# Performance work log

Measured on AMD Instinct MI355X. Metric: run time of the kernel, lower is better.

Reference implementation:

```python
import jax, jax.numpy as jnp
import numpy as np

EMBED = 1024
HEADS = 16
B, T = 2, 1024


def setup_inputs() -> dict:
    key = jax.random.key(0)
    k1, k2 = jax.random.split(key)
    x = jax.random.normal(k1, (B, T, EMBED), dtype=jnp.float32)
    # causal mask: True positions are masked to -inf (torch masked_fill semantics)
    mask = jnp.triu(jnp.ones((T, T), dtype=bool), k=1)
    weight = jax.random.normal(k2, (HEADS * EMBED, EMBED), dtype=jnp.float32)
    return {"x": x, "mask": mask, "weight": weight}


def reference(x, mask, weight):
    b, t, c = x.shape
    h = weight.shape[0] // c  # num_heads
    # split channels into heads: (b, h, t, head_dim)
    y = x.reshape(b, t, h, c // h).transpose(0, 2, 1, 3)
    # per-head scores (b, h, t, t)
    s = jnp.einsum('bhtk,bhsk->bhts', y, y)
    # mask BEFORE scaling, then scale by sqrt(num_heads) (not head_dim!)
    s = jnp.where(mask, -jnp.inf, s)
    p = jax.nn.softmax(s / jnp.sqrt(jnp.asarray(h, dtype=s.dtype)), axis=-1)
    # V is raw x broadcast across heads: (b, h, t, c)
    o = jnp.einsum('bhts,bsc->bhtc', p, x)
    # concat heads -> (b, t, h*c), final linear
    o = o.transpose(0, 2, 1, 3).reshape(b, t, h * c)
    return o @ weight
```

## Files before the change

kernel.cpp:

```cpp
#include <hip/hip_runtime.h>
#include <hip/hip_bf16.h>

#define B_ 2
#define T_ 1024
#define C_ 1024
#define H_ 16

typedef short bf16x8 __attribute__((ext_vector_type(8)));
typedef float f32x4 __attribute__((ext_vector_type(4)));

#define MFMA16(a, b, c) __builtin_amdgcn_mfma_f32_16x16x32_bf16(a, b, c, 0, 0, 0)

__device__ inline short f2bf(float x) {
    union { __hip_bfloat16 h; short s; } u;
    u.h = __float2bfloat16(x);
    return u.s;
}

__device__ inline void gl_lds16(const void* g, void* l) {
    __builtin_amdgcn_global_load_lds(
        (const __attribute__((address_space(1))) unsigned int*)g,
        (__attribute__((address_space(3))) unsigned int*)l, 16, 0, 0);
}

__global__ __launch_bounds__(256) void cvt_x(const float* __restrict__ x,
                                             short* __restrict__ xb) {
    int idx = (blockIdx.x * 256 + threadIdx.x) * 8;
    float4 a = *(const float4*)(x + idx);
    float4 b = *(const float4*)(x + idx + 4);
    bf16x8 v;
    v[0] = f2bf(a.x); v[1] = f2bf(a.y); v[2] = f2bf(a.z); v[3] = f2bf(a.w);
    v[4] = f2bf(b.x); v[5] = f2bf(b.y); v[6] = f2bf(b.z); v[7] = f2bf(b.w);
    *(bf16x8*)(xb + idx) = v;
}

__global__ __launch_bounds__(256) void cvt_w(const float* __restrict__ W,
                                             short* __restrict__ Wt) {
    __shared__ float T[64][65];
    const int bid = blockIdx.x;
    const int nb = bid & 15, cb = (bid >> 4) & 15, h = bid >> 8;
    const int t = threadIdx.x;
    const int c0 = cb * 64, n0 = nb * 64;
    const float* src = W + (size_t)(h * 1024 + c0) * 1024 + n0;
    {
        const int cl = t >> 4, nl = (t & 15) * 4;
#pragma unroll
        for (int r = 0; r < 4; ++r) {
            float4 v = *(const float4*)(src + (size_t)(cl + r * 16) * 1024 + nl);
            T[cl + r * 16][nl + 0] = v.x;
            T[cl + r * 16][nl + 1] = v.y;
            T[cl + r * 16][nl + 2] = v.z;
            T[cl + r * 16][nl + 3] = v.w;
        }
    }
    __syncthreads();
    {
        short* dst = Wt + (size_t)(h * 1024 + n0) * 1024 + c0;
        const int nl = t >> 3, cl8 = (t & 7) * 8;
#pragma unroll
        for (int r = 0; r < 2; ++r) {
            const int n = nl + r * 32;
            bf16x8 o;
#pragma unroll
            for (int j = 0; j < 8; ++j) o[j] = f2bf(T[cl8 + j][n]);
            *(bf16x8*)(dst + (size_t)n * 1024 + cl8) = o;
        }
    }
}

__global__ __launch_bounds__(512, 2) void attn_po(const short* __restrict__ xb,
                                                  const short* __restrict__ xbT,
                                                  short* __restrict__ O) {
    __shared__ short Pb[2][64][72];
    __shared__ float row_al[2][64];
    __shared__ float row_l[64];
    __shared__ int   flags[2][4];

    const int tid = threadIdx.x;
    const int bh = blockIdx.x & 31, p = blockIdx.x >> 5;
    const int b = bh >> 4, h = bh & 15;
    const int lane = tid & 63, q = lane >> 4, l16 = lane & 15;
    const int w = tid >> 6;
    const int g = w & 3;
    const int nw = w * 128;
    const short* xbb = xb + ((size_t)b << 20);
    const short* vtb = xbT + ((size_t)b << 20);

    const int tiles[2] = { p, 15 - p };
    for (int ti = 0; ti < 2; ++ti) {
        const int tb = tiles[ti];
        const int t0 = tb * 64;
        const int nch = tb + 1;

        f32x4 acc[4][8];
#pragma unroll
        for (int mt = 0; mt < 4; ++mt)
#pragma unroll
            for (int nt = 0; nt < 8; ++nt) acc[mt][nt] = (f32x4){0.f, 0.f, 0.f, 0.f};
        float m_r[4], l_r[4];
#pragma unroll
        for (int r = 0; r < 4; ++r) { m_r[r] = -3.0e38f; l_r[r] = 0.f; }

        bf16x8 qf[2];
        if (w < 4) {
#pragma unroll
            for (int ks = 0; ks < 2; ++ks)
                qf[ks] = *(const bf16x8*)(xbb + (size_t)(t0 + g * 16 + l16) * 1024 +
                                          h * 64 + ks * 32 + q * 8);
        }

        for (int ci = -1; ci < nch; ++ci) {
            __syncthreads();
            const int cc = ci + 1;
            if (w < 4 && cc < nch) {
                const int s0 = (cc == 0) ? t0 : (cc - 1) * 64;
                const int par = cc & 1;
                f32x4 sf[4];
#pragma unroll
                for (int st = 0; st < 4; ++st) sf[st] = (f32x4){0.f, 0.f, 0.f, 0.f};
#pragma unroll
                for (int st = 0; st < 4; ++st)
#pragma unroll
                    for (int ks = 0; ks < 2; ++ks) {
                        bf16x8 kf = *(const bf16x8*)(xbb +
                            (size_t)(s0 + st * 16 + l16) * 1024 + h * 64 + ks * 32 + q * 8);
                        sf[st] = MFMA16(qf[ks], kf, sf[st]);
                    }
                float mx[4] = {-3.0e38f, -3.0e38f, -3.0e38f, -3.0e38f};
#pragma unroll
                for (int st = 0; st < 4; ++st)
#pragma unroll
                    for (int r = 0; r < 4; ++r) {
                        float v = sf[st][r] * 0.25f;
                        if (cc == 0 && (s0 + st * 16 + l16) > (t0 + g * 16 + q * 4 + r))
                            v = -3.0e38f;
                        sf[st][r] = v;
                        mx[r] = fmaxf(mx[r], v);
                    }
#pragma unroll
                for (int r = 0; r < 4; ++r) {
                    mx[r] = fmaxf(mx[r], __shfl_xor(mx[r], 1));
                    mx[r] = fmaxf(mx[r], __shfl_xor(mx[r], 2));
                    mx[r] = fmaxf(mx[r], __shfl_xor(mx[r], 4));
                    mx[r] = fmaxf(mx[r], __shfl_xor(mx[r], 8));
                }
                float sum[4], al[4];
                int upd = 0;
#pragma unroll
                for (int r = 0; r < 4; ++r) {
                    float m_new = fmaxf(m_r[r], mx[r]);
                    al[r] = __expf(m_r[r] - m_new);
                    upd |= (m_new > m_r[r]) ? 1 : 0;
                    m_r[r] = m_new;
                    sum[r] = 0.f;
                }
#pragma unroll
                for (int st = 0; st < 4; ++st)
#pragma unroll
                    for (int r = 0; r < 4; ++r) {
                        float pv = __expf(sf[st][r] - m_r[r]);
                        sum[r] += pv;
                        Pb[par][g * 16 + q * 4 + r][st * 16 + l16] = f2bf(pv);
                    }
#pragma unroll
                for (int r = 0; r < 4; ++r) {
                    sum[r] += __shfl_xor(sum[r], 1);
                    sum[r] += __shfl_xor(sum[r], 2);
                    sum[r] += __shfl_xor(sum[r], 4);
                    sum[r] += __shfl_xor(sum[r], 8);
                    l_r[r] = l_r[r] * al[r] + sum[r];
                }
                if (l16 == 0) {
#pragma unroll
                    for (int r = 0; r < 4; ++r) row_al[par][g * 16 + q * 4 + r] = al[r];
                }
                int any_upd = __any(upd);
                if (lane == 0) flags[par][g] = any_upd;
            }
            if (ci >= 0) {
                const int par = ci & 1;
                if (flags[par][0] | flags[par][1] | flags[par][2] | flags[par][3]) {
#pragma unroll
                    for (int mt = 0; mt < 4; ++mt) {
                        float a0 = row_al[par][mt * 16 + q * 4 + 0];
                        float a1 = row_al[par][mt * 16 + q * 4 + 1];
                        float a2 = row_al[par][mt * 16 + q * 4 + 2];
                        float a3 = row_al[par][mt * 16 + q * 4 + 3];
#pragma unroll
                        for (int nt = 0; nt < 8; ++nt) {
                            acc[mt][nt][0] *= a0;
                            acc[mt][nt][1] *= a1;
                            acc[mt][nt][2] *= a2;
                            acc[mt][nt][3] *= a3;
                        }
                    }
                }
                bf16x8 pf[4][2];
#pragma unroll
                for (int mt = 0; mt < 4; ++mt)
#pragma unroll
                    for (int ks = 0; ks < 2; ++ks)
                        pf[mt][ks] = *(bf16x8*)&Pb[par][mt * 16 + l16][ks * 32 + q * 8];
                const int s0p = (ci == 0) ? t0 : (ci - 1) * 64;
#pragma unroll
                for (int nt = 0; nt < 8; ++nt)
#pragma unroll
                    for (int ks = 0; ks < 2; ++ks) {
                        bf16x8 vf = *(const bf16x8*)(vtb +
                            (size_t)(nw + nt * 16 + l16) * 1024 + s0p + ks * 32 + q * 8);
#pragma unroll
                        for (int mt = 0; mt < 4; ++mt)
                            acc[mt][nt] = MFMA16(pf[mt][ks], vf, acc[mt][nt]);
                    }
            }
        }

        if (w < 4 && l16 == 0) {
#pragma unroll
            for (int r = 0; r < 4; ++r) row_l[g * 16 + q * 4 + r] = l_r[r];
        }
        __syncthreads();
        short* ob = O + ((((size_t)(b * 1024 + t0) * 16) + h) << 10);
#pragma unroll
        for (int mt = 0; mt < 4; ++mt) {
            float i0 = 1.f / row_l[mt * 16 + q * 4 + 0];
            float i1 = 1.f / row_l[mt * 16 + q * 4 + 1];
            float i2 = 1.f / row_l[mt * 16 + q * 4 + 2];
            float i3 = 1.f / row_l[mt * 16 + q * 4 + 3];
#pragma unroll
            for (int nt = 0; nt < 8; ++nt) {
                size_t base = (size_t)(mt * 16 + q * 4) * 16384 + nw + nt * 16 + l16;
                ob[base]         = f2bf(acc[mt][nt][0] * i0);
                ob[base + 16384] = f2bf(acc[mt][nt][1] * i1);
                ob[base + 32768] = f2bf(acc[mt][nt][2] * i2);
                ob[base + 49152] = f2bf(acc[mt][nt][3] * i3);
            }
        }
        __syncthreads();
    }
}

__global__ __launch_bounds__(256, 4) void ogemm(const short* __restrict__ O,
                                                const short* __restrict__ Wt,
                                                float* __restrict__ out) {
    __shared__ short Al[4][128][8];
    __shared__ short Bl[4][128][8];

    const int bid = blockIdx.x;
    const int kq = bid >> 7, m_t = (bid >> 3) & 15, n_t = bid & 7;
    const int m0 = m_t * 128, n0 = n_t * 128;
    const int t = threadIdx.x;
    const int lane = t & 63, q = lane >> 4, l16 = lane & 15;
    const int wv = t >> 6;
    const int wm = (wv & 1) * 64, wn = (wv >> 1) * 64;

    const short* Ab = O + (size_t)m0 * 16384;
    const int srow = t & 127, skg = t >> 7;

    char* al_base = (char*)&Al[0][0][0] + (size_t)t * 16;
    char* bl_base = (char*)&Bl[0][0][0] + (size_t)t * 16;

    f32x4 acc[4][4];
#pragma unroll
    for (int i = 0; i < 4; ++i)
#pragma unroll
        for (int j = 0; j < 4; ++j) acc[i][j] = (f32x4){0.f, 0.f, 0.f, 0.f};

    const int kbase = kq * 4096;
    for (int kk = 0; kk < 4096; kk += 32) {
        const int k0 = kbase + kk;
        const int h = k0 >> 10, c0 = k0 & 1023;
        const short* Bb = Wt + ((size_t)h << 20) + (size_t)n0 * 1024 + c0;
        __syncthreads();
        gl_lds16(Ab + (size_t)srow * 16384 + k0 + skg * 8, al_base);
        gl_lds16(Ab + (size_t)srow * 16384 + k0 + (skg + 2) * 8, al_base + 4096);
        gl_lds16(Bb + (size_t)srow * 1024 + skg * 8, bl_base);
        gl_lds16(Bb + (size_t)srow * 1024 + (skg + 2) * 8, bl_base + 4096);
        __syncthreads();
        bf16x8 af[4], bfr[4];
#pragma unroll
        for (int i = 0; i < 4; ++i) af[i] = *(bf16x8*)&Al[q][wm + i * 16 + l16][0];
#pragma unroll
        for (int j = 0; j < 4; ++j) bfr[j] = *(bf16x8*)&Bl[q][wn + j * 16 + l16][0];
#pragma unroll
        for (int i = 0; i < 4; ++i)
#pragma unroll
            for (int j = 0; j < 4; ++j)
                acc[i][j] = MFMA16(af[i], bfr[j], acc[i][j]);
    }

#pragma unroll
    for (int i = 0; i < 4; ++i)
#pragma unroll
        for (int j = 0; j < 4; ++j)
#pragma unroll
            for (int r = 0; r < 4; ++r) {
                int m = m0 + wm + i * 16 + q * 4 + r;
                int n = n0 + wn + j * 16 + l16;
                atomicAdd(out + (size_t)m * 1024 + n, acc[i][j][r]);
            }
}

__global__ __launch_bounds__(256, 4) void zgemm_fast(const short* __restrict__ xb,
                                                     const short* __restrict__ Wt,
                                                     short* __restrict__ ZT) {
    __shared__ short Al[4][128][8];
    __shared__ short Bl[4][128][8];

    const int bid = blockIdx.x;
    const int n_t = bid & 7, h = (bid >> 3) & 15, s_t = bid >> 7;
    const int n0 = n_t * 128, s0g = s_t * 128;
    const int t = threadIdx.x;
    const int lane = t & 63, q = lane >> 4, l16 = lane & 15;
    const int wv = t >> 6;
    const int wm = (wv & 1) * 64, wn = (wv >> 1) * 64;

    const short* Ab = Wt + ((size_t)h * 1024 + n0) * 1024;
    const short* Bb = xb + (size_t)s0g * 1024;
    const int srow = t & 127, skg = t >> 7;

    char* al_base = (char*)&Al[0][0][0] + (size_t)t * 16;
    char* bl_base = (char*)&Bl[0][0][0] + (size_t)t * 16;

    f32x4 acc[4][4];
#pragma unroll
    for (int i = 0; i < 4; ++i)
#pragma unroll
        for (int j = 0; j < 4; ++j) acc[i][j] = (f32x4){0.f, 0.f, 0.f, 0.f};

    for (int k0 = 0; k0 < 1024; k0 += 32) {
        __syncthreads();
        gl_lds16(Ab + (size_t)srow * 1024 + k0 + skg * 8, al_base);
        gl_lds16(Ab + (size_t)srow * 1024 + k0 + (skg + 2) * 8, al_base + 4096);
        gl_lds16(Bb + (size_t)srow * 1024 + k0 + skg * 8, bl_base);
        gl_lds16(Bb + (size_t)srow * 1024 + k0 + (skg + 2) * 8, bl_base + 4096);
        __syncthreads();
        bf16x8 af[4], bfr[4];
#pragma unroll
        for (int i = 0; i < 4; ++i) af[i] = *(bf16x8*)&Al[q][wm + i * 16 + l16][0];
#pragma unroll
        for (int j = 0; j < 4; ++j) bfr[j] = *(bf16x8*)&Bl[q][wn + j * 16 + l16][0];
#pragma unroll
        for (int i = 0; i < 4; ++i)
#pragma unroll
            for (int j = 0; j < 4; ++j)
                acc[i][j] = MFMA16(af[i], bfr[j], acc[i][j]);
    }

    const int b = s0g >> 10, s_in0 = s0g & 1023;
    short* zb = ZT + ((size_t)(b * 16 + h) << 20);
#pragma unroll
    for (int i = 0; i < 4; ++i)
#pragma unroll
        for (int j = 0; j < 4; ++j)
#pragma unroll
            for (int r = 0; r < 4; ++r) {
                int n = n0 + wm + i * 16 + q * 4 + r;
                int s = s_in0 + wn + j * 16 + l16;
                zb[(size_t)n * 1024 + s] = f2bf(acc[i][j][r]);
            }
}

#define ZPAD 40

__global__ __launch_bounds__(256, 2) void zgemm_sm(const short* __restrict__ xb,
                                                   const float* __restrict__ W,
                                                   short* __restrict__ ZT) {
    __shared__ short Wts[128 * ZPAD];
    __shared__ short Xs[2][128 * ZPAD];

    const int tid = threadIdx.x;
    const int bs = blockIdx.x & 7;
    const int bn = (blockIdx.x >> 3) & 7;
    const int h  = blockIdx.x >> 6;
    const int s0 = bs * 128, n0 = bn * 128;
    const int lane = tid & 63, q = lane >> 4, l16 = lane & 15;
    const int w = tid >> 6, bw = w >> 1, sh = w & 1;

    f32x4 acc[8][4];
#pragma unroll
    for (int i = 0; i < 8; ++i)
#pragma unroll
        for (int j = 0; j < 4; ++j) acc[i][j] = (f32x4){0.f, 0.f, 0.f, 0.f};

    for (int k0 = 0; k0 < 1024; k0 += 32) {
        __syncthreads();
#pragma unroll
        for (int r = 0; r < 2; ++r) {
            const int c2 = ((tid >> 5) << 1) + (r << 4);
            const float* w0p = W + (size_t)(h * 1024 + k0 + c2) * 1024 + n0;
            const float* w1p = w0p + 1024;
#pragma unroll
            for (int i = 0; i < 4; ++i) {
                const int n = (tid & 31) + (i << 5);
                float wa = w0p[n], wb = w1p[n];
                unsigned u = (unsigned)(unsigned short)f2bf(wa) |
                             ((unsigned)(unsigned short)f2bf(wb) << 16);
                *(unsigned*)&Wts[n * ZPAD + c2] = u;
            }
        }
#pragma unroll
        for (int i = 0; i < 4; ++i) {
            const int id = tid + (i << 8);
            const int b2 = id >> 9, s = (id >> 2) & 127, cg = id & 3;
            bf16x8 v = *(const bf16x8*)(xb + (size_t)b2 * (T_ * C_) +
                                        (size_t)(s0 + s) * 1024 + k0 + cg * 8);
            *(bf16x8*)&Xs[b2][s * ZPAD + cg * 8] = v;
        }
        __syncthreads();

        bf16x8 af[8], bfr[4];
#pragma unroll
        for (int nt = 0; nt < 8; ++nt)
            af[nt] = *(bf16x8*)&Wts[(nt * 16 + l16) * ZPAD + q * 8];
#pragma unroll
        for (int st = 0; st < 4; ++st)
            bfr[st] = *(bf16x8*)&Xs[bw][(sh * 64 + st * 16 + l16) * ZPAD + q * 8];
#pragma unroll
        for (int nt = 0; nt < 8; ++nt)
#pragma unroll
            for (int st = 0; st < 4; ++st)
                acc[nt][st] = MFMA16(af[nt], bfr[st], acc[nt][st]);
    }

    short* zb = ZT + (size_t)(bw * 16 + h) * (1024 * 1024);
#pragma unroll
    for (int nt = 0; nt < 8; ++nt)
#pragma unroll
        for (int st = 0; st < 4; ++st)
#pragma unroll
            for (int r = 0; r < 4; ++r) {
                int n_abs = n0 + nt * 16 + q * 4 + r;
                int s_abs = s0 + sh * 64 + st * 16 + l16;
                zb[(size_t)n_abs * 1024 + s_abs] = f2bf(acc[nt][st][r]);
            }
}

__global__ __launch_bounds__(512, 2) void attn(const short* __restrict__ xb,
                                               const short* __restrict__ ZT,
                                               float* __restrict__ out) {
    __shared__ short Pb[2][64][72];
    __shared__ float row_al[2][64];
    __shared__ float row_l[64];
    __shared__ int   flags[2][4];

    const int tid = threadIdx.x;
    const int bh = blockIdx.x & 31, p = blockIdx.x >> 5;
    const int b = bh >> 4, h = bh & 15;
    const int lane = tid & 63, q = lane >> 4, l16 = lane & 15;
    const int w = tid >> 6;
    const int g = w & 3;
    const int nw = w * 128;
    const short* xbb = xb + ((size_t)b << 20);
    const short* ztb = ZT + ((size_t)(b * 16 + h) << 20);

    const int tiles[2] = { p, 15 - p };
    for (int ti = 0; ti < 2; ++ti) {
        const int tb = tiles[ti];
        const int t0 = tb * 64;
        const int nch = tb + 1;

        f32x4 acc[4][8];
#pragma unroll
        for (int mt = 0; mt < 4; ++mt)
#pragma unroll
            for (int nt = 0; nt < 8; ++nt) acc[mt][nt] = (f32x4){0.f, 0.f, 0.f, 0.f};
        float m_r[4], l_r[4];
#pragma unroll
        for (int r = 0; r < 4; ++r) { m_r[r] = -3.0e38f; l_r[r] = 0.f; }

        bf16x8 qf[2];
        if (w < 4) {
#pragma unroll
            for (int ks = 0; ks < 2; ++ks)
                qf[ks] = *(const bf16x8*)(xbb + (size_t)(t0 + g * 16 + l16) * 1024 +
                                          h * 64 + ks * 32 + q * 8);
        }

        for (int ci = -1; ci < nch; ++ci) {
            __syncthreads();
            const int cc = ci + 1;
            if (w < 4 && cc < nch) {
                const int s0 = (cc == 0) ? t0 : (cc - 1) * 64;
                const int par = cc & 1;
                f32x4 sf[4];
#pragma unroll
                for (int st = 0; st < 4; ++st) sf[st] = (f32x4){0.f, 0.f, 0.f, 0.f};
#pragma unroll
                for (int st = 0; st < 4; ++st)
#pragma unroll
                    for (int ks = 0; ks < 2; ++ks) {
                        bf16x8 kf = *(const bf16x8*)(xbb +
                            (size_t)(s0 + st * 16 + l16) * 1024 + h * 64 + ks * 32 + q * 8);
                        sf[st] = MFMA16(qf[ks], kf, sf[st]);
                    }
                float mx[4] = {-3.0e38f, -3.0e38f, -3.0e38f, -3.0e38f};
#pragma unroll
                for (int st = 0; st < 4; ++st)
#pragma unroll
                    for (int r = 0; r < 4; ++r) {
                        float v = sf[st][r] * 0.25f;
                        if (cc == 0 && (s0 + st * 16 + l16) > (t0 + g * 16 + q * 4 + r))
                            v = -3.0e38f;
                        sf[st][r] = v;
                        mx[r] = fmaxf(mx[r], v);
                    }
#pragma unroll
                for (int r = 0; r < 4; ++r) {
                    mx[r] = fmaxf(mx[r], __shfl_xor(mx[r], 1));
                    mx[r] = fmaxf(mx[r], __shfl_xor(mx[r], 2));
                    mx[r] = fmaxf(mx[r], __shfl_xor(mx[r], 4));
                    mx[r] = fmaxf(mx[r], __shfl_xor(mx[r], 8));
                }
                float sum[4], al[4];
                int upd = 0;
#pragma unroll
                for (int r = 0; r < 4; ++r) {
                    float m_new = fmaxf(m_r[r], mx[r]);
                    al[r] = __expf(m_r[r] - m_new);
                    upd |= (m_new > m_r[r]) ? 1 : 0;
                    m_r[r] = m_new;
                    sum[r] = 0.f;
                }
#pragma unroll
                for (int st = 0; st < 4; ++st)
#pragma unroll
                    for (int r = 0; r < 4; ++r) {
                        float pv = __expf(sf[st][r] - m_r[r]);
                        sum[r] += pv;
                        Pb[par][g * 16 + q * 4 + r][st * 16 + l16] = f2bf(pv);
                    }
#pragma unroll
                for (int r = 0; r < 4; ++r) {
                    sum[r] += __shfl_xor(sum[r], 1);
                    sum[r] += __shfl_xor(sum[r], 2);
                    sum[r] += __shfl_xor(sum[r], 4);
                    sum[r] += __shfl_xor(sum[r], 8);
                    l_r[r] = l_r[r] * al[r] + sum[r];
                }
                if (l16 == 0) {
#pragma unroll
                    for (int r = 0; r < 4; ++r) row_al[par][g * 16 + q * 4 + r] = al[r];
                }
                int any_upd = __any(upd);
                if (lane == 0) flags[par][g] = any_upd;
            }
            if (ci >= 0) {
                const int par = ci & 1;
                if (flags[par][0] | flags[par][1] | flags[par][2] | flags[par][3]) {
#pragma unroll
                    for (int mt = 0; mt < 4; ++mt) {
                        float a0 = row_al[par][mt * 16 + q * 4 + 0];
                        float a1 = row_al[par][mt * 16 + q * 4 + 1];
                        float a2 = row_al[par][mt * 16 + q * 4 + 2];
                        float a3 = row_al[par][mt * 16 + q * 4 + 3];
#pragma unroll
                        for (int nt = 0; nt < 8; ++nt) {
                            acc[mt][nt][0] *= a0;
                            acc[mt][nt][1] *= a1;
                            acc[mt][nt][2] *= a2;
                            acc[mt][nt][3] *= a3;
                        }
                    }
                }
                bf16x8 pf[4][2];
#pragma unroll
                for (int mt = 0; mt < 4; ++mt)
#pragma unroll
                    for (int ks = 0; ks < 2; ++ks)
                        pf[mt][ks] = *(bf16x8*)&Pb[par][mt * 16 + l16][ks * 32 + q * 8];
                const int s0p = (ci == 0) ? t0 : (ci - 1) * 64;
#pragma unroll
                for (int nt = 0; nt < 8; ++nt)
#pragma unroll
                    for (int ks = 0; ks < 2; ++ks) {
                        bf16x8 vf = *(const bf16x8*)(ztb +
                            (size_t)(nw + nt * 16 + l16) * 1024 + s0p + ks * 32 + q * 8);
#pragma unroll
                        for (int mt = 0; mt < 4; ++mt)
                            acc[mt][nt] = MFMA16(pf[mt][ks], vf, acc[mt][nt]);
                    }
            }
        }

        if (w < 4 && l16 == 0) {
#pragma unroll
            for (int r = 0; r < 4; ++r) row_l[g * 16 + q * 4 + r] = l_r[r];
        }
        __syncthreads();
#pragma unroll
        for (int mt = 0; mt < 4; ++mt) {
            float i0 = 1.f / row_l[mt * 16 + q * 4 + 0];
            float i1 = 1.f / row_l[mt * 16 + q * 4 + 1];
            float i2 = 1.f / row_l[mt * 16 + q * 4 + 2];
            float i3 = 1.f / row_l[mt * 16 + q * 4 + 3];
#pragma unroll
            for (int nt = 0; nt < 8; ++nt) {
                size_t base = (size_t)(b * 1024 + t0 + mt * 16 + q * 4) * 1024 +
                              nw + nt * 16 + l16;
                atomicAdd(out + base,            acc[mt][nt][0] * i0);
                atomicAdd(out + base + 1024,     acc[mt][nt][1] * i1);
                atomicAdd(out + base + 2048,     acc[mt][nt][2] * i2);
                atomicAdd(out + base + 3072,     acc[mt][nt][3] * i3);
            }
        }
        __syncthreads();
    }
}

extern "C" void kernel_launch(void* const* d_in, const int* in_sizes, int n_in,
                              void* d_out, int out_size, void* d_ws, size_t ws_size,
                              hipStream_t stream) {
    const float* x = (const float*)d_in[0];
    const float* W = (const float*)d_in[2];
    float* out = (float*)d_out;

    hipMemsetAsync(d_out, 0, (size_t)B_ * T_ * C_ * sizeof(float), stream);

    if (ws_size >= (size_t)104 * 1024 * 1024) {
        short* xb  = (short*)d_ws;
        short* xbT = xb + (size_t)2 * 1024 * 1024;
        short* Wt  = xb + (size_t)4 * 1024 * 1024;
        short* O   = xb + (size_t)20 * 1024 * 1024;

        cvt_x<<<(B_ * T_ * C_) / (256 * 8), 256, 0, stream>>>(x, xb);
        cvt_w<<<B_ * 16 * 16, 256, 0, stream>>>(x, xbT);
        cvt_w<<<16 * 16 * 16, 256, 0, stream>>>(W, Wt);
        attn_po<<<256, 512, 0, stream>>>(xb, xbT, O);
        ogemm<<<4 * 16 * 8, 256, 0, stream>>>(O, Wt, out);
    } else {
        short* xb = (short*)d_ws;
        short* ZT = (short*)d_ws + (size_t)B_ * T_ * C_;
        short* Wt = ZT + (size_t)B_ * H_ * 1024 * 1024;

        const bool big_ws = ws_size >= (size_t)100 * 1024 * 1024;
        cvt_x<<<(B_ * T_ * C_) / (256 * 8), 256, 0, stream>>>(x, xb);
        if (big_ws) {
            cvt_w<<<16 * 16 * 16, 256, 0, stream>>>(W, Wt);
            zgemm_fast<<<16 * 16 * 8, 256, 0, stream>>>(xb, Wt, ZT);
        } else {
            zgemm_sm<<<H_ * 8 * 8, 256, 0, stream>>>(xb, W, ZT);
        }
        attn<<<256, 512, 0, stream>>>(xb, ZT, out);
    }
}
```

Before: 374.4 us.

## Split attention tile pairs into separate blocks and deepen ogemm split-K

```diff
diff --git a/kernel.cpp b/kernel.cpp
--- a/kernel.cpp
+++ b/kernel.cpp
@@ -68,7 +68,7 @@
     }
 }
 
-__global__ __launch_bounds__(512, 2) void attn_po(const short* __restrict__ xb,
+__global__ __launch_bounds__(512, 4) void attn_po(const short* __restrict__ xb,
                                                   const short* __restrict__ xbT,
                                                   short* __restrict__ O) {
     __shared__ short Pb[2][64][72];
@@ -77,7 +77,9 @@
     __shared__ int   flags[2][4];
 
     const int tid = threadIdx.x;
-    const int bh = blockIdx.x & 31, p = blockIdx.x >> 5;
+    const int bh = blockIdx.x & 31;
+    const int rest = blockIdx.x >> 5;
+    const int tb = (rest < 8) ? rest : 23 - rest;
     const int b = bh >> 4, h = bh & 15;
     const int lane = tid & 63, q = lane >> 4, l16 = lane & 15;
     const int w = tid >> 6;
@@ -86,168 +88,166 @@
     const short* xbb = xb + ((size_t)b << 20);
     const short* vtb = xbT + ((size_t)b << 20);
 
-    const int tiles[2] = { p, 15 - p };
-    for (int ti = 0; ti < 2; ++ti) {
-        const int tb = tiles[ti];
-        const int t0 = tb * 64;
-        const int nch = tb + 1;
-
-        f32x4 acc[4][8];
-#pragma unroll
-        for (int mt = 0; mt < 4; ++mt)
-#pragma unroll
-            for (int nt = 0; nt < 8; ++nt) acc[mt][nt] = (f32x4){0.f, 0.f, 0.f, 0.f};
-        float m_r[4], l_r[4];
-#pragma unroll
-        for (int r = 0; r < 4; ++r) { m_r[r] = -3.0e38f; l_r[r] = 0.f; }
-
-        bf16x8 qf[2];
-        if (w < 4) {
-#pragma unroll
-            for (int ks = 0; ks < 2; ++ks)
-                qf[ks] = *(const bf16x8*)(xbb + (size_t)(t0 + g * 16 + l16) * 1024 +
-                                          h * 64 + ks * 32 + q * 8);
-        }
-
-        for (int ci = -1; ci < nch; ++ci) {
-            __syncthreads();
-            const int cc = ci + 1;
-            if (w < 4 && cc < nch) {
-                const int s0 = (cc == 0) ? t0 : (cc - 1) * 64;
-                const int par = cc & 1;
-                f32x4 sf[4];
-#pragma unroll
-                for (int st = 0; st < 4; ++st) sf[st] = (f32x4){0.f, 0.f, 0.f, 0.f};
-#pragma unroll
-                for (int st = 0; st < 4; ++st)
-#pragma unroll
-                    for (int ks = 0; ks < 2; ++ks) {
-                        bf16x8 kf = *(const bf16x8*)(xbb +
-                            (size_t)(s0 + st * 16 + l16) * 1024 + h * 64 + ks * 32 + q * 8);
-                        sf[st] = MFMA16(qf[ks], kf, sf[st]);
+    const int t0 = tb * 64;
+    const int nch = tb + 1;
+
+    f32x4 acc[4][8];
+#pragma unroll
+    for (int mt = 0; mt < 4; ++mt)
+#pragma unroll
+        for (int nt = 0; nt < 8; ++nt) acc[mt][nt] = (f32x4){0.f, 0.f, 0.f, 0.f};
+    float m_r[4], l_r[4];
+#pragma unroll
+    for (int r = 0; r < 4; ++r) { m_r[r] = -3.0e38f; l_r[r] = 0.f; }
+
+    bf16x8 qf[2];
+    if (w < 4) {
+#pragma unroll
+        for (int ks = 0; ks < 2; ++ks)
+            qf[ks] = *(const bf16x8*)(xbb + (size_t)(t0 + g * 16 + l16) * 1024 +
+                                      h * 64 + ks * 32 + q * 8);
+    }
+
+    for (int ci = -1; ci < nch; ++ci) {
+        __syncthreads();
+        const int cc = ci + 1;
+        if (w < 4 && cc < nch) {
+            const int s0 = (cc == 0) ? t0 : (cc - 1) * 64;
+            const int par = cc & 1;
+            f32x4 sf[4];
+#pragma unroll
+            for (int st = 0; st < 4; ++st) sf[st] = (f32x4){0.f, 0.f, 0.f, 0.f};
+#pragma unroll
+            for (int st = 0; st < 4; ++st)
+#pragma unroll
+                for (int ks = 0; ks < 2; ++ks) {
+                    bf16x8 kf = *(const bf16x8*)(xbb +
+                        (size_t)(s0 + st * 16 + l16) * 1024 + h * 64 + ks * 32 + q * 8);
+                    sf[st] = MFMA16(qf[ks], kf, sf[st]);
+                }
+            float mx[4] = {-3.0e38f, -3.0e38f, -3.0e38f, -3.0e38f};
+#pragma unroll
+            for (int st = 0; st < 4; ++st)
+#pragma unroll
+                for (int r = 0; r < 4; ++r) {
+                    float v = sf[st][r] * 0.25f;
+                    if (cc == 0 && (s0 + st * 16 + l16) > (t0 + g * 16 + q * 4 + r))
+                        v = -3.0e38f;
+                    sf[st][r] = v;
+                    mx[r] = fmaxf(mx[r], v);
+                }
+#pragma unroll
+            for (int r = 0; r < 4; ++r) {
+                mx[r] = fmaxf(mx[r], __shfl_xor(mx[r], 1));
+                mx[r] = fmaxf(mx[r], __shfl_xor(mx[r], 2));
+                mx[r] = fmaxf(mx[r], __shfl_xor(mx[r], 4));
+                mx[r] = fmaxf(mx[r], __shfl_xor(mx[r], 8));
+            }
+            float sum[4], al[4];
+            int upd = 0;
+#pragma unroll
+            for (int r = 0; r < 4; ++r) {
+                float m_new = fmaxf(m_r[r], mx[r]);
+                al[r] = __expf(m_r[r] - m_new);
+                upd |= (m_new > m_r[r]) ? 1 : 0;
+                m_r[r] = m_new;
+                sum[r] = 0.f;
+            }
+#pragma unroll
+            for (int st = 0; st < 4; ++st)
+#pragma unroll
+                for (int r = 0; r < 4; ++r) {
+                    float pv = __expf(sf[st][r] - m_r[r]);
+                    sum[r] += pv;
+                    Pb[par][g * 16 + q * 4 + r][st * 16 + l16] = f2bf(pv);
+                }
+#pragma unroll
+            for (int r = 0; r < 4; ++r) {
+                sum[r] += __shfl_xor(sum[r], 1);
+                sum[r] += __shfl_xor(sum[r], 2);
+                sum[r] += __shfl_xor(sum[r], 4);
+                sum[r] += __shfl_xor(sum[r], 8);
+                l_r[r] = l_r[r] * al[r] + sum[r];
+            }
+            if (l16 == 0) {
+#pragma unroll
+                for (int r = 0; r < 4; ++r) row_al[par][g * 16 + q * 4 + r] = al[r];
+            }
+            int any_upd = __any(upd);
+            if (lane == 0) flags[par][g] = any_upd;
+        }
+        if (ci >= 0) {
+            const int par = ci & 1;
+            if (flags[par][0] | flags[par][1] | flags[par][2] | flags[par][3]) {
+#pragma unroll
+                for (int mt = 0; mt < 4; ++mt) {
+                    float a0 = row_al[par][mt * 16 + q * 4 + 0];
+                    float a1 = row_al[par][mt * 16 + q * 4 + 1];
+                    float a2 = row_al[par][mt * 16 + q * 4 + 2];
+                    float a3 = row_al[par][mt * 16 + q * 4 + 3];
+#pragma unroll
+                    for (int nt = 0; nt < 8; ++nt) {
+                        acc[mt][nt][0] *= a0;
+                        acc[mt][nt][1] *= a1;
+                        acc[mt][nt][2] *= a2;
+                        acc[mt][nt][3] *= a3;
                     }
-                float mx[4] = {-3.0e38f, -3.0e38f, -3.0e38f, -3.0e38f};
-#pragma unroll
-                for (int st = 0; st < 4; ++st)
-#pragma unroll
-                    for (int r = 0; r < 4; ++r) {
-                        float v = sf[st][r] * 0.25f;
-                        if (cc == 0 && (s0 + st * 16 + l16) > (t0 + g * 16 + q * 4 + r))
-                            v = -3.0e38f;
-                        sf[st][r] = v;
-                        mx[r] = fmaxf(mx[r], v);
-                    }
-#pragma unroll
-                for (int r = 0; r < 4; ++r) {
-                    mx[r] = fmaxf(mx[r], __shfl_xor(mx[r], 1));
-                    mx[r] = fmaxf(mx[r], __shfl_xor(mx[r], 2));
-                    mx[r] = fmaxf(mx[r], __shfl_xor(mx[r], 4));
-                    mx[r] = fmaxf(mx[r], __shfl_xor(mx[r], 8));
-                }
-                float sum[4], al[4];
-                int upd = 0;
-#pragma unroll
-                for (int r = 0; r < 4; ++r) {
-                    float m_new = fmaxf(m_r[r], mx[r]);
-                    al[r] = __expf(m_r[r] - m_new);
-                    upd |= (m_new > m_r[r]) ? 1 : 0;
-                    m_r[r] = m_new;
-                    sum[r] = 0.f;
-                }
-#pragma unroll
-                for (int st = 0; st < 4; ++st)
-#pragma unroll
-                    for (int r = 0; r < 4; ++r) {
-                        float pv = __expf(sf[st][r] - m_r[r]);
-                        sum[r] += pv;
-                        Pb[par][g * 16 + q * 4 + r][st * 16 + l16] = f2bf(pv);
-                    }
-#pragma unroll
-                for (int r = 0; r < 4; ++r) {
-                    sum[r] += __shfl_xor(sum[r], 1);
-                    sum[r] += __shfl_xor(sum[r], 2);
-                    sum[r] += __shfl_xor(sum[r], 4);
-                    sum[r] += __shfl_xor(sum[r], 8);
-                    l_r[r] = l_r[r] * al[r] + sum[r];
-                }
-                if (l16 == 0) {
-#pragma unroll
-                    for (int r = 0; r < 4; ++r) row_al[par][g * 16 + q * 4 + r] = al[r];
-                }
-                int any_upd = __any(upd);
-                if (lane == 0) flags[par][g] = any_upd;
-            }
-            if (ci >= 0) {
-                const int par = ci & 1;
-                if (flags[par][0] | flags[par][1] | flags[par][2] | flags[par][3]) {
-#pragma unroll
-                    for (int mt = 0; mt < 4; ++mt) {
-                        float a0 = row_al[par][mt * 16 + q * 4 + 0];
-                        float a1 = row_al[par][mt * 16 + q * 4 + 1];
-                        float a2 = row_al[par][mt * 16 + q * 4 + 2];
-                        float a3 = row_al[par][mt * 16 + q * 4 + 3];
-#pragma unroll
-                        for (int nt = 0; nt < 8; ++nt) {
-                            acc[mt][nt][0] *= a0;
-                            acc[mt][nt][1] *= a1;
-                            acc[mt][nt][2] *= a2;
-                            acc[mt][nt][3] *= a3;
-                        }
-                    }
-                }
-                bf16x8 pf[4][2];
-#pragma unroll
-                for (int mt = 0; mt < 4; ++mt)
-#pragma unroll
-                    for (int ks = 0; ks < 2; ++ks)
-                        pf[mt][ks] = *(bf16x8*)&Pb[par][mt * 16 + l16][ks * 32 + q * 8];
-                const int s0p = (ci == 0) ? t0 : (ci - 1) * 64;
-#pragma unroll
-                for (int nt = 0; nt < 8; ++nt)
-#pragma unroll
-                    for (int ks = 0; ks < 2; ++ks) {
-                        bf16x8 vf = *(const bf16x8*)(vtb +
-                            (size_t)(nw + nt * 16 + l16) * 1024 + s0p + ks * 32 + q * 8);
-#pragma unroll
-                        for (int mt = 0; mt < 4; ++mt)
-                            acc[mt][nt] = MFMA16(pf[mt][ks], vf, acc[mt][nt]);
-                    }
-            }
-        }
-
-        if (w < 4 && l16 == 0) {
-#pragma unroll
-            for (int r = 0; r < 4; ++r) row_l[g * 16 + q * 4 + r] = l_r[r];
-        }
-        __syncthreads();
-        short* ob = O + ((((size_t)(b * 1024 + t0) * 16) + h) << 10);
-#pragma unroll
-        for (int mt = 0; mt < 4; ++mt) {
-            float i0 = 1.f / row_l[mt * 16 + q * 4 + 0];
-            float i1 = 1.f / row_l[mt * 16 + q * 4 + 1];
-            float i2 = 1.f / row_l[mt * 16 + q * 4 + 2];
-            float i3 = 1.f / row_l[mt * 16 + q * 4 + 3];
-#pragma unroll
-            for (int nt = 0; nt < 8; ++nt) {
-                size_t base = (size_t)(mt * 16 + q * 4) * 16384 + nw + nt * 16 + l16;
-                ob[base]         = f2bf(acc[mt][nt][0] * i0);
-                ob[base + 16384] = f2bf(acc[mt][nt][1] * i1);
-                ob[base + 32768] = f2bf(acc[mt][nt][2] * i2);
-                ob[base + 49152] = f2bf(acc[mt][nt][3] * i3);
-            }
-        }
-        __syncthreads();
+                }
+            }
+            bf16x8 pf[4][2];
+#pragma unroll
+            for (int mt = 0; mt < 4; ++mt)
+#pragma unroll
+                for (int ks = 0; ks < 2; ++ks)
+                    pf[mt][ks] = *(bf16x8*)&Pb[par][mt * 16 + l16][ks * 32 + q * 8];
+            const int s0p = (ci == 0) ? t0 : (ci - 1) * 64;
+#pragma unroll
+            for (int nt = 0; nt < 8; ++nt)
+#pragma unroll
+                for (int ks = 0; ks < 2; ++ks) {
+                    bf16x8 vf = *(const bf16x8*)(vtb +
+                        (size_t)(nw + nt * 16 + l16) * 1024 + s0p + ks * 32 + q * 8);
+#pragma unroll
+                    for (int mt = 0; mt < 4; ++mt)
+                        acc[mt][nt] = MFMA16(pf[mt][ks], vf, acc[mt][nt]);
+                }
+        }
+    }
+
+    if (w < 4 && l16 == 0) {
+#pragma unroll
+        for (int r = 0; r < 4; ++r) row_l[g * 16 + q * 4 + r] = l_r[r];
+    }
+    __syncthreads();
+    short* ob = O + ((((size_t)(b * 1024 + t0) * 16) + h) << 10);
+#pragma unroll
+    for (int mt = 0; mt < 4; ++mt) {
+        float i0 = 1.f / row_l[mt * 16 + q * 4 + 0];
+        float i1 = 1.f / row_l[mt * 16 + q * 4 + 1];
+        float i2 = 1.f / row_l[mt * 16 + q * 4 + 2];
+        float i3 = 1.f / row_l[mt * 16 + q * 4 + 3];
+#pragma unroll
+        for (int nt = 0; nt < 8; ++nt) {
+            size_t base = (size_t)(mt * 16 + q * 4) * 16384 + nw + nt * 16 + l16;
+            ob[base]         = f2bf(acc[mt][nt][0] * i0);
+            ob[base + 16384] = f2bf(acc[mt][nt][1] * i1);
+            ob[base + 32768] = f2bf(acc[mt][nt][2] * i2);
+            ob[base + 49152] = f2bf(acc[mt][nt][3] * i3);
+        }
     }
 }
 
 __global__ __launch_bounds__(256, 4) void ogemm(const short* __restrict__ O,
                                                 const short* __restrict__ Wt,
                                                 float* __restrict__ out) {
-    __shared__ short Al[4][128][8];
-    __shared__ short Bl[4][128][8];
-
-    const int bid = blockIdx.x;
-    const int kq = bid >> 7, m_t = (bid >> 3) & 15, n_t = bid & 7;
+    __shared__ short Al[8][128][8];
+    __shared__ short Bl[8][128][8];
+
+    const int orig = blockIdx.x;
+    const int wgid = (orig & 7) * 128 + (orig >> 3);
+    const int kq  = wgid >> 7;
+    const int m_t = (wgid >> 3) & 15;
+    const int n_t = wgid & 7;
     const int m0 = m_t * 128, n0 = n_t * 128;
     const int t = threadIdx.x;
     const int lane = t & 63, q = lane >> 4, l16 = lane & 15;
@@ -266,27 +266,34 @@
 #pragma unroll
         for (int j = 0; j < 4; ++j) acc[i][j] = (f32x4){0.f, 0.f, 0.f, 0.f};
 
-    const int kbase = kq * 4096;
-    for (int kk = 0; kk < 4096; kk += 32) {
+    const int kbase = kq << 11;
+    for (int kk = 0; kk < 2048; kk += 64) {
         const int k0 = kbase + kk;
         const int h = k0 >> 10, c0 = k0 & 1023;
-        const short* Bb = Wt + ((size_t)h << 20) + (size_t)n0 * 1024 + c0;
-        __syncthreads();
-        gl_lds16(Ab + (size_t)srow * 16384 + k0 + skg * 8, al_base);
-        gl_lds16(Ab + (size_t)srow * 16384 + k0 + (skg + 2) * 8, al_base + 4096);
-        gl_lds16(Bb + (size_t)srow * 1024 + skg * 8, bl_base);
-        gl_lds16(Bb + (size_t)srow * 1024 + (skg + 2) * 8, bl_base + 4096);
-        __syncthreads();
-        bf16x8 af[4], bfr[4];
-#pragma unroll
-        for (int i = 0; i < 4; ++i) af[i] = *(bf16x8*)&Al[q][wm + i * 16 + l16][0];
-#pragma unroll
-        for (int j = 0; j < 4; ++j) bfr[j] = *(bf16x8*)&Bl[q][wn + j * 16 + l16][0];
-#pragma unroll
-        for (int i = 0; i < 4; ++i)
+        const short* Arow = Ab + (size_t)srow * 16384 + k0;
+        const short* Brow = Wt + ((size_t)h << 20) + (size_t)(n0 + srow) * 1024 + c0;
+        __syncthreads();
+#pragma unroll
+        for (int j = 0; j < 4; ++j) {
+            gl_lds16(Arow + (2 * j + skg) * 8, al_base + j * 4096);
+            gl_lds16(Brow + (2 * j + skg) * 8, bl_base + j * 4096);
+        }
+        __syncthreads();
+#pragma unroll
+        for (int ks = 0; ks < 2; ++ks) {
+            bf16x8 af[4], bfr[4];
+#pragma unroll
+            for (int i = 0; i < 4; ++i)
+                af[i] = *(bf16x8*)&Al[q + 4 * ks][wm + i * 16 + l16][0];
 #pragma unroll
             for (int j = 0; j < 4; ++j)
-                acc[i][j] = MFMA16(af[i], bfr[j], acc[i][j]);
+                bfr[j] = *(bf16x8*)&Bl[q + 4 * ks][wn + j * 16 + l16][0];
+#pragma unroll
+            for (int i = 0; i < 4; ++i)
+#pragma unroll
+                for (int j = 0; j < 4; ++j)
+                    acc[i][j] = MFMA16(af[i], bfr[j], acc[i][j]);
+        }
     }
 
 #pragma unroll
@@ -626,8 +633,8 @@
         cvt_x<<<(B_ * T_ * C_) / (256 * 8), 256, 0, stream>>>(x, xb);
         cvt_w<<<B_ * 16 * 16, 256, 0, stream>>>(x, xbT);
         cvt_w<<<16 * 16 * 16, 256, 0, stream>>>(W, Wt);
-        attn_po<<<256, 512, 0, stream>>>(xb, xbT, O);
-        ogemm<<<4 * 16 * 8, 256, 0, stream>>>(O, Wt, out);
+        attn_po<<<512, 512, 0, stream>>>(xb, xbT, O);
+        ogemm<<<1024, 256, 0, stream>>>(O, Wt, out);
     } else {
         short* xb = (short*)d_ws;
         short* ZT = (short*)d_ws + (size_t)B_ * T_ * C_;
```

Result: slower. 679.6 us (+81.5%).
